# Kernel tuning notes

Measured on AMD Instinct MI355X. Metric: run time of the kernel, lower is better.

## Reference

```python
import jax, jax.numpy as jnp
import numpy as np
import math

V = 50257   # target_vocab_size
E = 512     # opt.out_embeddings_size
B = 8
L = 2048
NR = 100    # noise_ratio
NORM_TERM = math.log(V)   # norm_term='auto'
LOG_NR = math.log(NR)


def setup_inputs() -> dict:
    key = jax.random.key(0)
    k1, k2, k3, k4, k5 = jax.random.split(key, 5)
    # build_unigram_noise: counts -> probs; clamp(1e-10); renorm; log  (Zipf-like counts)
    counts = 1.0 / np.arange(1, V + 1, dtype=np.float64)
    probs = counts / counts.sum()
    probs = np.clip(probs, 1e-10, None)
    probs = probs / probs.sum()
    logprob_noise = jnp.asarray(np.log(probs), dtype=jnp.float32)
    target = jax.random.randint(k1, (B, L), 0, V)
    noise_idx = jax.random.randint(k2, (NR,), 0, V)  # shared noise (per_word=False)
    inp = jax.random.normal(k3, (B, L, E), jnp.float32) * 0.05
    emb_weight = jax.random.normal(k4, (V, E), jnp.float32) * 0.02
    bias_weight = jax.random.normal(k5, (V,), jnp.float32) * 0.01
    return {"input": inp, "emb_weight": emb_weight, "bias_weight": bias_weight,
            "logprob_noise": logprob_noise, "target": target, "noise_idx": noise_idx}


def reference(input, emb_weight, bias_weight, logprob_noise, target, noise_idx):
    # _compute_sampled_logit_batched
    flat_in = input.reshape(-1, E)                    # (B*L, E)
    tflat = target.reshape(-1)                        # (B*L,)
    t_emb = emb_weight[tflat]                         # gather (B*L, E)
    target_score = jnp.sum(flat_in * t_emb, axis=1) + bias_weight[tflat]
    n_emb = emb_weight[noise_idx]                     # (NR, E)
    noise_score = flat_in @ n_emb.T + bias_weight[noise_idx]  # (B*L, NR)
    # _get_logit: subtract norm term
    logit_t_model = target_score.reshape(B, L) - NORM_TERM
    logit_n_model = noise_score.reshape(B, L, NR) - NORM_TERM
    # noise-distribution log-probs
    logit_t_noise = logprob_noise[target]                                   # (B, L)
    logit_n_noise = jnp.broadcast_to(logprob_noise[noise_idx], (B, L, NR))  # shared
    # nce_loss
    logit_model = jnp.concatenate([logit_t_model[..., None], logit_n_model], axis=2)
    logit_noise = jnp.concatenate([logit_t_noise[..., None], logit_n_noise], axis=2)
    x = logit_model - logit_noise - LOG_NR            # (B, L, NR+1)
    # BCEWithLogits, label=1 at slot 0 else 0: loss = softplus(x) - x*y
    bce = jnp.logaddexp(0.0, x)
    bce = bce.at[:, :, 0].add(-x[:, :, 0])
    loss = bce.sum(axis=2)                            # (B, L)
    return loss.mean()                                # reduction='elementwise_mean'
```

## Files before the change

### kernel.cpp

```cpp
#include <hip/hip_runtime.h>


#define E_SZ   512
#define NROWS  16384
#define NRn    100
#define NWp    112
#define MT     16
#define NBLK   (NROWS / MT)

typedef __attribute__((ext_vector_type(8))) short short8;
typedef __attribute__((ext_vector_type(4))) float f32x4;

#define NTL 15.430077572997398f

__device__ __forceinline__ unsigned int pack2(float a, float b) {
    unsigned int ua = __float_as_uint(a) + 0x8000u;
    unsigned int ub = __float_as_uint(b) + 0x8000u;
    return __builtin_amdgcn_perm(ub, ua, 0x07060302u);
}
__device__ __forceinline__ short8 cvt8(float4 x0, float4 x1) {
    union { unsigned int u[4]; short8 s; } r;
    r.u[0] = pack2(x0.x, x0.y);
    r.u[1] = pack2(x0.z, x0.w);
    r.u[2] = pack2(x1.x, x1.y);
    r.u[3] = pack2(x1.z, x1.w);
    return r.s;
}
__device__ __forceinline__ float softplus(float x) {
    return fmaxf(x, 0.f) + log1pf(__expf(-fabsf(x)));
}

__global__ __launch_bounds__(128)
void prep_noise(const float* __restrict__ emb, const float* __restrict__ bias,
                const float* __restrict__ lpn, const int* __restrict__ nidx,
                unsigned short* __restrict__ nB,
                float* __restrict__ nBn)
{
    const int j = blockIdx.x;
    const int t = threadIdx.x;
    const int idx = (j < NRn) ? nidx[j] : 0;
    float4 v = {0.f, 0.f, 0.f, 0.f};
    if (j < NRn) v = *(const float4*)(emb + (size_t)idx * E_SZ + t * 4);
    union { unsigned int u[2]; } r;
    r.u[0] = pack2(v.x, v.y);
    r.u[1] = pack2(v.z, v.w);
    *(uint2*)(nB + (size_t)j * E_SZ + t * 4) = make_uint2(r.u[0], r.u[1]);
    if (t == 0)
        nBn[j] = (j < NRn) ? (bias[idx] - NTL - lpn[idx]) : 0.f;
}

__global__ __launch_bounds__(256, 4)
void nce_loss_kernel(const float* __restrict__ inp,
                     const float* __restrict__ emb,
                     const float* __restrict__ bias,
                     const float* __restrict__ lpn,
                     const int*   __restrict__ target,
                     const unsigned short* __restrict__ nB,
                     const float* __restrict__ nBn,
                     float* __restrict__ out)
{
    const int t    = threadIdx.x;
    const int w    = t >> 6;
    const int lane = t & 63;
    const int c    = lane & 15;
    const int q    = lane >> 4;
    const int r0   = blockIdx.x * MT;

    __shared__ float sAcc[4 * 2048];
    __shared__ float sBn[NWp];
    __shared__ float sTb[MT];
    __shared__ float sWs[4];

    if (t < NWp) sBn[t] = nBn[t];
    if (t < MT) {
        int tg = target[r0 + t];
        sTb[t] = bias[tg] - NTL - lpn[tg];
    }

    const float* pA = inp + (size_t)(r0 + c) * E_SZ;
    const float* pT = emb + (size_t)target[r0 + c] * E_SZ;
    const unsigned short* pN[7];
#pragma unroll
    for (int ti = 0; ti < 7; ++ti)
        pN[ti] = nB + (size_t)(ti * 16 + c) * E_SZ;

    f32x4 accN[7];
    f32x4 accT = {0.f, 0.f, 0.f, 0.f};
#pragma unroll
    for (int ti = 0; ti < 7; ++ti) accN[ti] = {0.f, 0.f, 0.f, 0.f};

    const int kb = w * 128 + q * 8;

#define LOADSTEP(K)                                          \
    {                                                        \
        curA[0] = *(const float4*)(pA + (K));                \
        curA[1] = *(const float4*)(pA + (K) + 4);            \
        curT[0] = *(const float4*)(pT + (K));                \
        curT[1] = *(const float4*)(pT + (K) + 4);            \
        _Pragma("unroll")                                    \
        for (int ti = 0; ti < 7; ++ti)                       \
            curB[ti] = *(const short8*)(pN[ti] + (K));       \
    }

    float4 curA[2], curT[2];
    short8 curB[7];
    LOADSTEP(kb);

#pragma unroll
    for (int ks = 0; ks < 4; ++ks) {
        short8 A = cvt8(curA[0], curA[1]);
        short8 T = cvt8(curT[0], curT[1]);
        short8 Bv[7];
#pragma unroll
        for (int ti = 0; ti < 7; ++ti) Bv[ti] = curB[ti];

        if (ks < 3) LOADSTEP(kb + (ks + 1) * 32);

        accT = __builtin_amdgcn_mfma_f32_16x16x32_bf16(A, T, accT, 0, 0, 0);
#pragma unroll
        for (int ti = 0; ti < 7; ++ti)
            accN[ti] = __builtin_amdgcn_mfma_f32_16x16x32_bf16(A, Bv[ti], accN[ti], 0, 0, 0);
    }
#undef LOADSTEP

    float* slab = sAcc + w * 2048;
#pragma unroll
    for (int ti = 0; ti < 7; ++ti)
#pragma unroll
        for (int r = 0; r < 4; ++r)
            slab[ti * 256 + r * 64 + lane] = accN[ti][r];
#pragma unroll
    for (int r = 0; r < 4; ++r)
        slab[7 * 256 + r * 64 + lane] = accT[r];
    __syncthreads();

    const int ereg = w;
    const int col  = lane & 15;
    const int erow = (lane >> 4) * 4 + ereg;
    float ll = 0.f;
#pragma unroll
    for (int i = 0; i < 7; ++i) {
        int word = i * 16 + col;
        float v = sAcc[i * 256 + t] + sAcc[2048 + i * 256 + t]
                + sAcc[4096 + i * 256 + t] + sAcc[6144 + i * 256 + t];
        if (word < NRn)
            ll += softplus(v + sBn[word]);
    }
    {
        float v = sAcc[7 * 256 + t] + sAcc[2048 + 7 * 256 + t]
                + sAcc[4096 + 7 * 256 + t] + sAcc[6144 + 7 * 256 + t];
        if (col == erow)
            ll += softplus(-(v + sTb[erow]));
    }

#pragma unroll
    for (int off = 32; off > 0; off >>= 1) ll += __shfl_down(ll, off);
    if (lane == 0) sWs[w] = ll;
    __syncthreads();
    if (t == 0) {
        float s = (sWs[0] + sWs[1]) + (sWs[2] + sWs[3]);
        atomicAdd(out, s * (1.f / (float)NROWS));
    }
}

extern "C" void kernel_launch(void* const* d_in, const int* in_sizes, int n_in,
                              void* d_out, int out_size, void* d_ws, size_t ws_size,
                              hipStream_t stream) {
    const float* inp    = (const float*)d_in[0];
    const float* emb    = (const float*)d_in[1];
    const float* bias   = (const float*)d_in[2];
    const float* lpn    = (const float*)d_in[3];
    const int*   target = (const int*)d_in[4];
    const int*   nidx   = (const int*)d_in[5];
    float* out = (float*)d_out;

    unsigned short* nB  = (unsigned short*)d_ws;
    float*          nBn = (float*)((char*)d_ws + (size_t)NWp * E_SZ * 2);

    hipMemsetAsync(out, 0, sizeof(float), stream);
    prep_noise<<<NWp, 128, 0, stream>>>(emb, bias, lpn, nidx, nB, nBn);
    nce_loss_kernel<<<NBLK, 256, 0, stream>>>(inp, emb, bias, lpn, target, nB, nBn, out);
}
```

Measured before the change: 185.0 us.

## Interleave noise bf16 matrix by k-group and prefetch all A/T loads upfront

```diff
diff --git a/kernel.cpp b/kernel.cpp
--- a/kernel.cpp
+++ b/kernel.cpp
@@ -18,6 +18,9 @@
     unsigned int ub = __float_as_uint(b) + 0x8000u;
     return __builtin_amdgcn_perm(ub, ua, 0x07060302u);
 }
+__device__ __forceinline__ float softplus(float x) {
+    return fmaxf(x, 0.f) + log1pf(__expf(-fabsf(x)));
+}
 __device__ __forceinline__ short8 cvt8(float4 x0, float4 x1) {
     union { unsigned int u[4]; short8 s; } r;
     r.u[0] = pack2(x0.x, x0.y);
@@ -25,9 +28,6 @@
     r.u[2] = pack2(x1.x, x1.y);
     r.u[3] = pack2(x1.z, x1.w);
     return r.s;
-}
-__device__ __forceinline__ float softplus(float x) {
-    return fmaxf(x, 0.f) + log1pf(__expf(-fabsf(x)));
 }
 
 __global__ __launch_bounds__(128)
@@ -41,15 +41,16 @@
     const int idx = (j < NRn) ? nidx[j] : 0;
     float4 v = {0.f, 0.f, 0.f, 0.f};
     if (j < NRn) v = *(const float4*)(emb + (size_t)idx * E_SZ + t * 4);
-    union { unsigned int u[2]; } r;
-    r.u[0] = pack2(v.x, v.y);
-    r.u[1] = pack2(v.z, v.w);
-    *(uint2*)(nB + (size_t)j * E_SZ + t * 4) = make_uint2(r.u[0], r.u[1]);
+    unsigned int u0 = pack2(v.x, v.y);
+    unsigned int u1 = pack2(v.z, v.w);
+    const int kg  = t >> 1;
+    const int off = (t & 1) * 4;
+    *(uint2*)(nB + ((size_t)kg * NWp + j) * 8 + off) = make_uint2(u0, u1);
     if (t == 0)
         nBn[j] = (j < NRn) ? (bias[idx] - NTL - lpn[idx]) : 0.f;
 }
 
-__global__ __launch_bounds__(256, 4)
+__global__ __launch_bounds__(256, 3)
 void nce_loss_kernel(const float* __restrict__ inp,
                      const float* __restrict__ emb,
                      const float* __restrict__ bias,
@@ -77,51 +78,49 @@
         sTb[t] = bias[tg] - NTL - lpn[tg];
     }
 
-    const float* pA = inp + (size_t)(r0 + c) * E_SZ;
-    const float* pT = emb + (size_t)target[r0 + c] * E_SZ;
-    const unsigned short* pN[7];
-#pragma unroll
-    for (int ti = 0; ti < 7; ++ti)
-        pN[ti] = nB + (size_t)(ti * 16 + c) * E_SZ;
+    const int kb = w * 128 + q * 8;
+    const float* pA = inp + (size_t)(r0 + c) * E_SZ + kb;
+    const float* pT = emb + (size_t)target[r0 + c] * E_SZ + kb;
+    const unsigned short* pB = nB + ((size_t)(w * 16 + q) * NWp + c) * 8;
 
     f32x4 accN[7];
     f32x4 accT = {0.f, 0.f, 0.f, 0.f};
 #pragma unroll
     for (int ti = 0; ti < 7; ++ti) accN[ti] = {0.f, 0.f, 0.f, 0.f};
 
-    const int kb = w * 128 + q * 8;
+    short8 curB[7];
+#pragma unroll
+    for (int ti = 0; ti < 7; ++ti) curB[ti] = *(const short8*)(pB + ti * 128);
 
-#define LOADSTEP(K)                                          \
-    {                                                        \
-        curA[0] = *(const float4*)(pA + (K));                \
-        curA[1] = *(const float4*)(pA + (K) + 4);            \
-        curT[0] = *(const float4*)(pT + (K));                \
-        curT[1] = *(const float4*)(pT + (K) + 4);            \
-        _Pragma("unroll")                                    \
-        for (int ti = 0; ti < 7; ++ti)                       \
-            curB[ti] = *(const short8*)(pN[ti] + (K));       \
+    float4 a[4][2], tt[4][2];
+#pragma unroll
+    for (int ks = 0; ks < 4; ++ks) {
+        a[ks][0]  = *(const float4*)(pA + ks * 32);
+        a[ks][1]  = *(const float4*)(pA + ks * 32 + 4);
+        tt[ks][0] = *(const float4*)(pT + ks * 32);
+        tt[ks][1] = *(const float4*)(pT + ks * 32 + 4);
     }
-
-    float4 curA[2], curT[2];
-    short8 curB[7];
-    LOADSTEP(kb);
 
 #pragma unroll
     for (int ks = 0; ks < 4; ++ks) {
-        short8 A = cvt8(curA[0], curA[1]);
-        short8 T = cvt8(curT[0], curT[1]);
+        short8 A = cvt8(a[ks][0], a[ks][1]);
+        short8 T = cvt8(tt[ks][0], tt[ks][1]);
         short8 Bv[7];
 #pragma unroll
         for (int ti = 0; ti < 7; ++ti) Bv[ti] = curB[ti];
 
-        if (ks < 3) LOADSTEP(kb + (ks + 1) * 32);
+        if (ks < 3) {
+            const unsigned short* pBn = pB + (ks + 1) * 4 * NWp * 8;
+#pragma unroll
+            for (int ti = 0; ti < 7; ++ti)
+                curB[ti] = *(const short8*)(pBn + ti * 128);
+        }
 
         accT = __builtin_amdgcn_mfma_f32_16x16x32_bf16(A, T, accT, 0, 0, 0);
 #pragma unroll
         for (int ti = 0; ti < 7; ++ti)
             accN[ti] = __builtin_amdgcn_mfma_f32_16x16x32_bf16(A, Bv[ti], accN[ti], 0, 0, 0);
     }
-#undef LOADSTEP
 
     float* slab = sAcc + w * 2048;
 #pragma unroll
@@ -175,7 +174,7 @@
     float* out = (float*)d_out;
 
     unsigned short* nB  = (unsigned short*)d_ws;
-    float*          nBn = (float*)((char*)d_ws + (size_t)NWp * E_SZ * 2);
+    float*          nBn = (float*)((char*)d_ws + (size_t)64 * NWp * 8 * 2);
 
     hipMemsetAsync(out, 0, sizeof(float), stream);
     prep_noise<<<NWp, 128, 0, stream>>>(emb, bias, lpn, nidx, nB, nBn);
```

Measured after the change: 178.4 us. 1.04x faster.
